# Kernel optimization log

Hardware: AMD Instinct MI355X
Metric: run time of the kernel (lower is better)

The kernel has to match this reference:

```python
import jax, jax.numpy as jnp
import numpy as np

N_NODES = 50000

def cheb_conv(x, edge_index, W, b):
    # PyG ChebConv, K=2, normalization='sym', lambda_max=2.0 (default):
    # scaled Laplacian L_hat = (2/lambda_max)*L - I = -D^{-1/2} A D^{-1/2} (zero diag).
    # Tx_0 = x, Tx_1 = L_hat @ x ; out = Tx_0 @ W[0] + Tx_1 @ W[1] + b
    src, dst = edge_index[0], edge_index[1]
    ones = jnp.ones(src.shape[0], x.dtype)
    deg = jax.ops.segment_sum(ones, src, num_segments=N_NODES)
    dinv = jnp.where(deg > 0, 1.0 / jnp.sqrt(deg), 0.0)
    norm = -dinv[src] * dinv[dst]                                   # [E]
    tx1 = jax.ops.segment_sum(x[src] * norm[:, None], dst, num_segments=N_NODES)
    return x @ W[0] + tx1 @ W[1] + b

def setup_inputs() -> dict:
    key = jax.random.key(0)
    ks = jax.random.split(key, 12)
    IN, OUT, E, P = 128, 2, 800000, 400000
    return {
        "x": jax.random.normal(ks[0], (N_NODES, IN), jnp.float32),
        "edge_index": jax.random.randint(ks[1], (2, E), 0, N_NODES),
        "E_pos": jax.random.randint(ks[2], (2, P), 0, N_NODES),
        "neg_edge_index": jax.random.randint(ks[3], (2, P), 0, N_NODES),
        "W1": jax.random.normal(ks[4], (2, IN, 300), jnp.float32) * 0.05,
        "b1": jnp.zeros((300,), jnp.float32),
        "W2": jax.random.normal(ks[5], (2, 300, 100), jnp.float32) * 0.05,
        "b2": jnp.zeros((100,), jnp.float32),
        "W3": jax.random.normal(ks[6], (2, 100, OUT), jnp.float32) * 0.05,
        "b3": jnp.zeros((OUT,), jnp.float32),
        "lin1_W": jax.random.normal(ks[7], (100, IN), jnp.float32) * 0.05,
        "lin1_b": jnp.zeros((100,), jnp.float32),
        "lin2_W": jax.random.normal(ks[8], (100, IN), jnp.float32) * 0.05,
        "lin2_b": jnp.zeros((100,), jnp.float32),
        "c1": jnp.full((1,), 0.5, jnp.float32),
        "c2": jnp.full((1,), 0.5, jnp.float32),
    }

def reference(x, edge_index, E_pos, neg_edge_index, W1, b1, W2, b2, W3, b3,
              lin1_W, lin1_b, lin2_W, lin2_b, c1, c2):
    # eval mode: F.dropout and dropout_edge are identity
    x0 = x
    h = jax.nn.relu(cheb_conv(x0, edge_index, W1, b1))
    x1 = jax.nn.relu(cheb_conv(h, edge_index, W2, b2))
    x2 = x1 + jax.nn.relu(x0 @ lin1_W.T + lin1_b)
    z = x1 + jax.nn.relu(x0 @ lin2_W.T + lin2_b)
    pos_score = jnp.sum(z[E_pos[0]] * z[E_pos[1]], axis=1)              # [P]
    pos_loss = -jnp.mean(jnp.log(jax.nn.sigmoid(pos_score) + 1e-15))
    neg_score = jnp.sum(z[neg_edge_index[0]] * z[neg_edge_index[1]], axis=1)
    neg_loss = -jnp.mean(jnp.log(1.0 - jax.nn.sigmoid(neg_score) + 1e-15))
    r_loss = pos_loss + neg_loss
    out = cheb_conv(x2, edge_index, W3, b3)                             # [N, out_channels]
    return (out, r_loss, c1, c2)
```

## Files before the change

### kernel.cpp

```cpp
#include <hip/hip_runtime.h>
#include <math.h>


typedef unsigned short ushort_t;
typedef unsigned char u8;
typedef __attribute__((ext_vector_type(8))) __bf16 bf16x8;
typedef __attribute__((ext_vector_type(8))) short s16x8;
typedef __attribute__((ext_vector_type(4))) float f32x4;
typedef __attribute__((ext_vector_type(2))) float f32x2;

#define NB_H 256
#define HW 12500
#define PW 25000
#define LOSS_NB 1792

__device__ __forceinline__ f32x4 mfma16x16x32(s16x8 a, s16x8 b, f32x4 c) {
  return __builtin_amdgcn_mfma_f32_16x16x32_bf16(
      __builtin_bit_cast(bf16x8, a), __builtin_bit_cast(bf16x8, b), c, 0, 0, 0);
}
__device__ __forceinline__ ushort_t f2bf(float f) {
  union { float f; unsigned u; } c; c.f = f;
  unsigned r = (c.u + 0x7FFFu + ((c.u >> 16) & 1u)) >> 16;
  return (ushort_t)r;
}
__device__ __forceinline__ f32x2 cvt2lo(unsigned u) {
  return __builtin_amdgcn_cvt_pk_f32_fp8((int)u, false);
}
__device__ __forceinline__ f32x2 cvt2hi(unsigned u) {
  return __builtin_amdgcn_cvt_pk_f32_fp8((int)u, true);
}
__device__ __forceinline__ u8 f2fp8(float f) {
  return (u8)(__builtin_amdgcn_cvt_pk_fp8_f32(f, 0.f, 0, false) & 0xff);
}

template<int VAR, int NT, int KTOT>
__global__ __launch_bounds__(256) void gemm_mfma(
    const ushort_t* __restrict__ A0, const ushort_t* __restrict__ A1,
    const ushort_t* __restrict__ Wt,
    const float* __restrict__ bias0, const float* __restrict__ bias1,
    const float* __restrict__ x1,
    const float* __restrict__ W3c, const float* __restrict__ b3c,
    void* __restrict__ out0, void* __restrict__ out1,
    float* __restrict__ t0g, float* __restrict__ t1g, int M)
{
  constexpr int NF = NT / 32;
  __shared__ __align__(16) ushort_t As[64 * 40];
  __shared__ __align__(16) ushort_t Bs[NT * 40];
  __shared__ float w3s[400];
  const int tid  = threadIdx.x;
  const int lane = tid & 63, w = tid >> 6;
  const int m0 = blockIdx.x * 64;
  const int wm = (w & 1) * 32, wn = (w >> 1) * (NT / 2);
  if (VAR == 2) { for (int i = tid; i < 400; i += 256) w3s[i] = W3c[i]; }
  f32x4 acc[2][NF];
#pragma unroll
  for (int i = 0; i < 2; ++i)
#pragma unroll
    for (int j = 0; j < NF; ++j) acc[i][j] = (f32x4){0.f, 0.f, 0.f, 0.f};

  for (int k0 = 0; k0 < KTOT; k0 += 32) {
    {
      const int r = tid >> 2, c8 = (tid & 3) * 8;
      const int gm = m0 + r;
      uint4 v = {0u, 0u, 0u, 0u};
      if (gm < M) {
        if (VAR == 1) {
          const u8* s8 = (const u8*)A0 + (size_t)gm * 320 + k0 + c8;
          const uint2 r8 = *(const uint2*)s8;
          const f32x2 f0 = cvt2lo(r8.x), f1 = cvt2hi(r8.x);
          const f32x2 f2 = cvt2lo(r8.y), f3 = cvt2hi(r8.y);
          v.x = (unsigned)f2bf(f0.x) | ((unsigned)f2bf(f0.y) << 16);
          v.y = (unsigned)f2bf(f1.x) | ((unsigned)f2bf(f1.y) << 16);
          v.z = (unsigned)f2bf(f2.x) | ((unsigned)f2bf(f2.y) << 16);
          v.w = (unsigned)f2bf(f3.x) | ((unsigned)f2bf(f3.y) << 16);
        } else {
          const ushort_t* srcp;
          if (VAR == 0) srcp = (k0 < 128) ? A0 + (size_t)gm * 128 + k0 + c8
                                          : A1 + (size_t)gm * 128 + (k0 - 128) + c8;
          else srcp = A0 + (size_t)gm * 128 + k0 + c8;
          v = *(const uint4*)srcp;
        }
      }
      *(uint4*)&As[r * 40 + c8] = v;
    }
    {
      const int c8 = (tid & 3) * 8;
#pragma unroll
      for (int i = 0; i < (NT * 4 + 255) / 256; ++i) {
        const int r = (tid >> 2) + i * 64;
        if (r < NT)
          *(uint4*)&Bs[r * 40 + c8] = *(const uint4*)(Wt + (size_t)r * KTOT + k0 + c8);
      }
    }
    __syncthreads();
    s16x8 af[2], bfr[NF];
#pragma unroll
    for (int mi = 0; mi < 2; ++mi)
      af[mi] = *(const s16x8*)&As[(wm + mi * 16 + (lane & 15)) * 40 + (lane >> 4) * 8];
#pragma unroll
    for (int ni = 0; ni < NF; ++ni)
      bfr[ni] = *(const s16x8*)&Bs[(wn + ni * 16 + (lane & 15)) * 40 + (lane >> 4) * 8];
#pragma unroll
    for (int mi = 0; mi < 2; ++mi)
#pragma unroll
      for (int ni = 0; ni < NF; ++ni)
        acc[mi][ni] = mfma16x16x32(af[mi], bfr[ni], acc[mi][ni]);
    __syncthreads();
  }

  if (VAR == 2) {
#pragma unroll
    for (int mi = 0; mi < 2; ++mi)
#pragma unroll
      for (int r = 0; r < 4; ++r) {
        const int gRow = m0 + wm + mi * 16 + ((lane >> 4) << 2) + r;
        float p0 = 0.f, p1 = 0.f, p2 = 0.f, p3 = 0.f;
#pragma unroll
        for (int ni = 0; ni < NF; ++ni) {
          const int col = wn + ni * 16 + (lane & 15);
          const float v = acc[mi][ni][r];
          if (gRow < M) {
            if (col < 100) {
              const float x2v = x1[(size_t)gRow * 128 + col] + fmaxf(v + bias0[col], 0.f);
              p0 = fmaf(x2v, w3s[col * 2 + 0], p0);
              p1 = fmaf(x2v, w3s[col * 2 + 1], p1);
              p2 = fmaf(x2v, w3s[200 + col * 2 + 0], p2);
              p3 = fmaf(x2v, w3s[200 + col * 2 + 1], p3);
            } else if (col < 200) {
              const int c = col - 100;
              ((u8*)out1)[(size_t)gRow * 128 + c] =
                  f2fp8(x1[(size_t)gRow * 128 + c] + fmaxf(v + bias1[c], 0.f));
            }
          }
        }
        if (wn == 0) {
#pragma unroll
          for (int off = 8; off; off >>= 1) {
            p0 += __shfl_down(p0, off, 16);
            p1 += __shfl_down(p1, off, 16);
            p2 += __shfl_down(p2, off, 16);
            p3 += __shfl_down(p3, off, 16);
          }
          if ((lane & 15) == 0 && gRow < M) {
            t0g[(size_t)gRow * 2 + 0] = p0 + b3c[0];
            t0g[(size_t)gRow * 2 + 1] = p1 + b3c[1];
            t1g[(size_t)gRow * 2 + 0] = p2;
            t1g[(size_t)gRow * 2 + 1] = p3;
          }
        }
      }
  } else {
#pragma unroll
    for (int mi = 0; mi < 2; ++mi)
#pragma unroll
      for (int ni = 0; ni < NF; ++ni)
#pragma unroll
        for (int r = 0; r < 4; ++r) {
          const int gRow = m0 + wm + mi * 16 + ((lane >> 4) << 2) + r;
          const int col  = wn + ni * 16 + (lane & 15);
          if (gRow >= M) continue;
          const float v = acc[mi][ni][r];
          if (VAR == 0) {
            ((u8*)out0)[(size_t)gRow * 320 + col] =
                (col < 300) ? f2fp8(fmaxf(v + bias0[col], 0.f)) : (u8)0;
          } else {
            if (col < 100) ((float*)out0)[(size_t)gRow * 128 + col] = v + bias0[col];
            else if (col < 200) ((u8*)out1)[(size_t)gRow * 128 + (col - 100)] = f2fp8(v);
          }
        }
  }
}

__global__ __launch_bounds__(256) void prep(
    const int* __restrict__ src, const int* __restrict__ dst, int E, int M,
    unsigned* __restrict__ partS, unsigned* __restrict__ partD,
    ushort_t* __restrict__ rank,
    const float* __restrict__ x, ushort_t* __restrict__ xb,
    u8* __restrict__ xf8, int n4,
    const float* __restrict__ W1, const float* __restrict__ W2,
    const float* __restrict__ l1W, const float* __restrict__ l2W,
    ushort_t* __restrict__ W1t, ushort_t* __restrict__ W2t,
    ushort_t* __restrict__ Wlt)
{
  __shared__ unsigned hist[HW];
  const int blk = blockIdx.x;
  if (blk < 512) {
    const int isD = (blk >= 256);
    const int b = isD ? blk - 256 : blk;
    const int* keys = isD ? dst : src;
    unsigned* part = isD ? partD : partS;
    const int cs = (E + NB_H - 1) / NB_H;
    const int e0 = b * cs;
    const int e1 = (e0 + cs < E) ? e0 + cs : E;
    for (int r = 0; r < 2; ++r) {
      const int klo = r * 2 * HW;
      for (int i = threadIdx.x; i < HW; i += 256) hist[i] = 0;
      __syncthreads();
      for (int e = e0 + threadIdx.x; e < e1; e += 256) {
        const int k = keys[e] - klo;
        if ((unsigned)k < (unsigned)(2 * HW)) {
          const unsigned old = atomicAdd(&hist[k >> 1], (k & 1) ? 0x10000u : 1u);
          if (isD) rank[e] = (ushort_t)((old >> ((k & 1) * 16)) & 0xffffu);
        }
      }
      __syncthreads();
      for (int i = threadIdx.x; i < HW; i += 256)
        part[(size_t)b * PW + r * HW + i] = hist[i];
      __syncthreads();
    }
    return;
  }
  const int i = (blk - 512) * 256 + threadIdx.x;
  if (i < n4) {
    const float4 v = ((const float4*)x)[i];
    ushort4 o; o.x = f2bf(v.x); o.y = f2bf(v.y); o.z = f2bf(v.z); o.w = f2bf(v.w);
    ((ushort4*)xb)[i] = o;
    int p = 0;
    p = __builtin_amdgcn_cvt_pk_fp8_f32(v.x, v.y, p, false);
    p = __builtin_amdgcn_cvt_pk_fp8_f32(v.z, v.w, p, true);
    ((unsigned*)xf8)[i] = (unsigned)p;
    return;
  }
  const int j = i - n4;
  if (j < 81920) {
    const int n = j >> 8, k = j & 255;
    float v = 0.f;
    if (n < 300) v = (k < 128) ? W1[k * 300 + n] : W1[38400 + (k - 128) * 300 + n];
    W1t[j] = f2bf(v);
  } else if (j < 153600) {
    const int jj = j - 81920;
    const int n = jj / 320, k = jj - n * 320;
    float v = 0.f;
    if (n < 200 && k < 300) v = W2[(n < 100 ? 0 : 30000) + k * 100 + (n % 100)];
    W2t[jj] = f2bf(v);
  } else if (j < 182272) {
    const int jj = j - 153600;
    const int n = jj >> 7, k = jj & 127;
    float v = 0.f;
    if (n < 100) v = l1W[n * 128 + k];
    else if (n < 200) v = l2W[(n - 100) * 128 + k];
    Wlt[jj] = f2bf(v);
  }
}

__global__ __launch_bounds__(256) void reduce_base2(
    const unsigned* __restrict__ partS, unsigned* __restrict__ partD,
    float* __restrict__ dinv, int* __restrict__ cnt, int M)
{
  const int t = blockIdx.x * 256 + threadIdx.x;
  if (t < PW) {
    const int i = t;
    unsigned ssum = 0;
    for (int b = 0; b < NB_H; b += 8) {
      unsigned v[8];
#pragma unroll
      for (int q = 0; q < 8; ++q) v[q] = partS[(size_t)(b + q) * PW + i];
#pragma unroll
      for (int q = 0; q < 8; ++q) ssum += v[q];
    }
    const int k = 2 * i;
    const unsigned s0 = ssum & 0xffffu, s1 = ssum >> 16;
    if (k < M) dinv[k] = s0 ? 1.f / sqrtf((float)s0) : 0.f;
    if (k + 1 < M) dinv[k + 1] = s1 ? 1.f / sqrtf((float)s1) : 0.f;
  } else if (t < 2 * PW) {
    const int i = t - PW;
    unsigned run = 0;
    for (int b = 0; b < NB_H; b += 8) {
      unsigned v[8], pre[8];
#pragma unroll
      for (int q = 0; q < 8; ++q) v[q] = partD[(size_t)(b + q) * PW + i];
#pragma unroll
      for (int q = 0; q < 8; ++q) { pre[q] = run; run += v[q]; }
#pragma unroll
      for (int q = 0; q < 8; ++q) partD[(size_t)(b + q) * PW + i] = pre[q];
    }
    const int k = 2 * i;
    if (k < M) cnt[k] = (int)(run & 0xffffu);
    if (k + 1 < M) cnt[k + 1] = (int)(run >> 16);
  }
}

__global__ void scan_local(const int* __restrict__ cnt, int* __restrict__ ptr,
                           int* __restrict__ bsum, int n)
{
  __shared__ int tmp[256];
  const int i = blockIdx.x * 256 + threadIdx.x;
  const int v = (i < n) ? cnt[i] : 0;
  tmp[threadIdx.x] = v;
  __syncthreads();
  for (int off = 1; off < 256; off <<= 1) {
    const int t = (threadIdx.x >= off) ? tmp[threadIdx.x - off] : 0;
    __syncthreads();
    tmp[threadIdx.x] += t;
    __syncthreads();
  }
  if (i < n) ptr[i] = tmp[threadIdx.x] - v;
  if (threadIdx.x == 255) bsum[blockIdx.x] = tmp[255];
}
__global__ void scan_add2(int* __restrict__ ptr, const int* __restrict__ bsum,
                          int n, int E, int nb, float* __restrict__ accs)
{
  __shared__ int tmp[256];
  const int v = (threadIdx.x < nb) ? bsum[threadIdx.x] : 0;
  tmp[threadIdx.x] = v;
  __syncthreads();
  for (int off = 1; off < 256; off <<= 1) {
    const int t = (threadIdx.x >= off) ? tmp[threadIdx.x - off] : 0;
    __syncthreads();
    tmp[threadIdx.x] += t;
    __syncthreads();
  }
  __syncthreads();
  const int offset = (blockIdx.x > 0) ? tmp[blockIdx.x - 1] : 0;
  const int i = blockIdx.x * 256 + threadIdx.x;
  if (i < n) ptr[i] += offset;
  if (i == 0) { ptr[n] = E; accs[0] = 0.f; accs[1] = 0.f; }
}

__global__ void fill_csr2(const int* __restrict__ src, const int* __restrict__ dst,
                          const float* __restrict__ dinv, const int* __restrict__ ptr,
                          const unsigned* __restrict__ base32,
                          const ushort_t* __restrict__ rank,
                          int2* __restrict__ csr, int E)
{
  const int e = blockIdx.x * 256 + threadIdx.x;
  if (e >= E) return;
  const int cs = (E + NB_H - 1) / NB_H;
  const int b = e / cs;
  const int s = src[e], d = dst[e];
  const unsigned bv = base32[(size_t)b * PW + (d >> 1)];
  const int base = (int)((bv >> ((d & 1) * 16)) & 0xffffu);
  const int pos = ptr[d] + base + (int)rank[e];
  const float w = -dinv[s] * dinv[d];
  csr[pos] = make_int2(s, __float_as_int(w));
}

#define ACCV(u, ww) { f32x2 t; \
  t = cvt2lo(u.x); a[0]  = fmaf(ww, t.x, a[0]);  a[1]  = fmaf(ww, t.y, a[1]);  \
  t = cvt2hi(u.x); a[2]  = fmaf(ww, t.x, a[2]);  a[3]  = fmaf(ww, t.y, a[3]);  \
  t = cvt2lo(u.y); a[4]  = fmaf(ww, t.x, a[4]);  a[5]  = fmaf(ww, t.y, a[5]);  \
  t = cvt2hi(u.y); a[6]  = fmaf(ww, t.x, a[6]);  a[7]  = fmaf(ww, t.y, a[7]);  \
  t = cvt2lo(u.z); a[8]  = fmaf(ww, t.x, a[8]);  a[9]  = fmaf(ww, t.y, a[9]);  \
  t = cvt2hi(u.z); a[10] = fmaf(ww, t.x, a[10]); a[11] = fmaf(ww, t.y, a[11]); \
  t = cvt2lo(u.w); a[12] = fmaf(ww, t.x, a[12]); a[13] = fmaf(ww, t.y, a[13]); \
  t = cvt2hi(u.w); a[14] = fmaf(ww, t.x, a[14]); a[15] = fmaf(ww, t.y, a[15]); }

__global__ __launch_bounds__(256) void gather128e(
    const u8* __restrict__ xf8, ushort_t* __restrict__ txb,
    const int* __restrict__ ptr, const int2* __restrict__ csr, int M)
{
  const int node = (blockIdx.x * 256 + threadIdx.x) >> 3;
  const int sub  = threadIdx.x & 7;
  if (node >= M) return;
  const int beg = ptr[node], end = ptr[node + 1];
  float a[16] = {};
  int p = beg;
  for (; p + 8 <= end; p += 8) {
    int2 e[8];
#pragma unroll
    for (int q = 0; q < 8; ++q) e[q] = csr[p + q];
    uint4 v[8];
#pragma unroll
    for (int q = 0; q < 8; ++q)
      v[q] = *(const uint4*)(xf8 + (size_t)e[q].x * 128 + sub * 16);
#pragma unroll
    for (int q = 0; q < 8; ++q) { const float wq = __int_as_float(e[q].y); ACCV(v[q], wq) }
  }
  for (; p < end; ++p) {
    const int2 eq = csr[p]; const float wq = __int_as_float(eq.y);
    const uint4 v = *(const uint4*)(xf8 + (size_t)eq.x * 128 + sub * 16);
    ACCV(v, wq)
  }
  uint4 o1, o2;
  o1.x = (unsigned)f2bf(a[0])  | ((unsigned)f2bf(a[1])  << 16);
  o1.y = (unsigned)f2bf(a[2])  | ((unsigned)f2bf(a[3])  << 16);
  o1.z = (unsigned)f2bf(a[4])  | ((unsigned)f2bf(a[5])  << 16);
  o1.w = (unsigned)f2bf(a[6])  | ((unsigned)f2bf(a[7])  << 16);
  o2.x = (unsigned)f2bf(a[8])  | ((unsigned)f2bf(a[9])  << 16);
  o2.y = (unsigned)f2bf(a[10]) | ((unsigned)f2bf(a[11]) << 16);
  o2.z = (unsigned)f2bf(a[12]) | ((unsigned)f2bf(a[13]) << 16);
  o2.w = (unsigned)f2bf(a[14]) | ((unsigned)f2bf(a[15]) << 16);
  ushort_t* dstp = txb + (size_t)node * 128 + sub * 16;
  *(uint4*)dstp = o1;
  *(uint4*)(dstp + 8) = o2;
}

__global__ __launch_bounds__(256) void gather100e_x1(
    const u8* __restrict__ Brh, float* __restrict__ Ar,
    const int* __restrict__ ptr, const int2* __restrict__ csr, int M)
{
  const int node = (blockIdx.x * 256 + threadIdx.x) >> 3;
  const int sub  = threadIdx.x & 7;
  if (node >= M) return;
  const int beg = ptr[node], end = ptr[node + 1];
  float a[16] = {};
  int p = beg;
  for (; p + 8 <= end; p += 8) {
    int2 e[8];
#pragma unroll
    for (int q = 0; q < 8; ++q) e[q] = csr[p + q];
    uint4 v[8];
#pragma unroll
    for (int q = 0; q < 8; ++q)
      v[q] = *(const uint4*)(Brh + (size_t)e[q].x * 128 + sub * 16);
#pragma unroll
    for (int q = 0; q < 8; ++q) { const float wq = __int_as_float(e[q].y); ACCV(v[q], wq) }
  }
  for (; p < end; ++p) {
    const int2 eq = csr[p]; const float wq = __int_as_float(eq.y);
    const uint4 v = *(const uint4*)(Brh + (size_t)eq.x * 128 + sub * 16);
    ACCV(v, wq)
  }
  float* dstp = Ar + (size_t)node * 128 + sub * 16;
#pragma unroll
  for (int q = 0; q < 4; ++q) {
    float4 b = *(const float4*)(dstp + q * 4);
    b.x = fmaxf(b.x + a[q * 4 + 0], 0.f);
    b.y = fmaxf(b.y + a[q * 4 + 1], 0.f);
    b.z = fmaxf(b.z + a[q * 4 + 2], 0.f);
    b.w = fmaxf(b.w + a[q * 4 + 3], 0.f);
    *(float4*)(dstp + q * 4) = b;
  }
}
#undef ACCV

__device__ __forceinline__ void maskrow(uint4& r, int sub) {
  if (sub >= 6) { r.y = 0u; r.z = 0u; r.w = 0u; if (sub == 7) r.x = 0u; }
}
#define DOTV(uu, vv, s) { f32x2 p_, q_; \
  p_ = cvt2lo(uu.x); q_ = cvt2lo(vv.x); s = fmaf(p_.x, q_.x, s); s = fmaf(p_.y, q_.y, s); \
  p_ = cvt2hi(uu.x); q_ = cvt2hi(vv.x); s = fmaf(p_.x, q_.x, s); s = fmaf(p_.y, q_.y, s); \
  p_ = cvt2lo(uu.y); q_ = cvt2lo(vv.y); s = fmaf(p_.x, q_.x, s); s = fmaf(p_.y, q_.y, s); \
  p_ = cvt2hi(uu.y); q_ = cvt2hi(vv.y); s = fmaf(p_.x, q_.x, s); s = fmaf(p_.y, q_.y, s); \
  p_ = cvt2lo(uu.z); q_ = cvt2lo(vv.z); s = fmaf(p_.x, q_.x, s); s = fmaf(p_.y, q_.y, s); \
  p_ = cvt2hi(uu.z); q_ = cvt2hi(vv.z); s = fmaf(p_.x, q_.x, s); s = fmaf(p_.y, q_.y, s); \
  p_ = cvt2lo(uu.w); q_ = cvt2lo(vv.w); s = fmaf(p_.x, q_.x, s); s = fmaf(p_.y, q_.y, s); \
  p_ = cvt2hi(uu.w); q_ = cvt2hi(vv.w); s = fmaf(p_.x, q_.x, s); s = fmaf(p_.y, q_.y, s); }

__global__ __launch_bounds__(256) void loss_g2(
    const u8* __restrict__ zf8, const int* __restrict__ ep,
    const int* __restrict__ en, int P, float* __restrict__ acc,
    const float* __restrict__ t1, const float* __restrict__ t0,
    const int* __restrict__ ptr, const int2* __restrict__ csr,
    float* __restrict__ out, int M)
{
  const int tid = threadIdx.x;
  if (blockIdx.x >= LOSS_NB) {
    const int i = (blockIdx.x - LOSS_NB) * 256 + tid;
    if (i >= M) return;
    float a0 = 0.f, a1 = 0.f;
    const int beg = ptr[i], end = ptr[i + 1];
    int p = beg;
    for (; p + 4 <= end; p += 4) {
      const int2 e0 = csr[p], e1 = csr[p + 1], e2 = csr[p + 2], e3 = csr[p + 3];
      const float w0 = __int_as_float(e0.y), w1 = __int_as_float(e1.y);
      const float w2 = __int_as_float(e2.y), w3 = __int_as_float(e3.y);
      const float2 v0 = *(const float2*)(t1 + (size_t)e0.x * 2);
      const float2 v1 = *(const float2*)(t1 + (size_t)e1.x * 2);
      const float2 v2 = *(const float2*)(t1 + (size_t)e2.x * 2);
      const float2 v3 = *(const float2*)(t1 + (size_t)e3.x * 2);
      a0 = fmaf(w0, v0.x, a0); a1 = fmaf(w0, v0.y, a1);
      a0 = fmaf(w1, v1.x, a0); a1 = fmaf(w1, v1.y, a1);
      a0 = fmaf(w2, v2.x, a0); a1 = fmaf(w2, v2.y, a1);
      a0 = fmaf(w3, v3.x, a0); a1 = fmaf(w3, v3.y, a1);
    }
    for (; p < end; ++p) {
      const int2 eq = csr[p]; const float wq = __int_as_float(eq.y);
      const float2 v = *(const float2*)(t1 + (size_t)eq.x * 2);
      a0 = fmaf(wq, v.x, a0); a1 = fmaf(wq, v.y, a1);
    }
    const float2 base = *(const float2*)(t0 + (size_t)i * 2);
    *(float2*)(out + (size_t)i * 2) = make_float2(base.x + a0, base.y + a1);
    return;
  }
  __shared__ float red[8];
  const int lane = tid & 63, wib = tid >> 6;
  const int sub = tid & 7;
  const int slot0 = blockIdx.x * 32 + (tid >> 3);
  const int step = LOSS_NB * 32;
  float tp = 0.f, tn = 0.f;
  int g = slot0;
  for (; g + 3 * step < 2 * P; g += 4 * step) {
    int neg[4], na[4], nb[4];
#pragma unroll
    for (int q = 0; q < 4; ++q) {
      const int gq = g + q * step;
      neg[q] = (gq >= P);
      const int p = neg[q] ? gq - P : gq;
      const int* ia = neg[q] ? en : ep;
      na[q] = ia[p]; nb[q] = ia[P + p];
    }
    uint4 ra[4], rb[4];
#pragma unroll
    for (int q = 0; q < 4; ++q) {
      ra[q] = make_uint4(0u, 0u, 0u, 0u);
      rb[q] = make_uint4(0u, 0u, 0u, 0u);
      if (sub < 7) {
        ra[q] = *(const uint4*)(zf8 + (size_t)na[q] * 128 + sub * 16);
        rb[q] = *(const uint4*)(zf8 + (size_t)nb[q] * 128 + sub * 16);
      }
      maskrow(ra[q], sub); maskrow(rb[q], sub);
    }
    float s[4] = {0.f, 0.f, 0.f, 0.f};
#pragma unroll
    for (int q = 0; q < 4; ++q) DOTV(ra[q], rb[q], s[q])
#pragma unroll
    for (int off = 4; off; off >>= 1) {
#pragma unroll
      for (int q = 0; q < 4; ++q) s[q] += __shfl_down(s[q], off, 8);
    }
    if (sub == 0) {
#pragma unroll
      for (int q = 0; q < 4; ++q) {
        const float sig = 1.f / (1.f + __expf(-s[q]));
        if (neg[q]) tn += __logf(1.f - sig + 1e-15f); else tp += __logf(sig + 1e-15f);
      }
    }
  }
  for (; g < 2 * P; g += step) {
    const int neg = (g >= P);
    const int p = neg ? g - P : g;
    const int* ia = neg ? en : ep;
    const int na = ia[p], nb = ia[P + p];
    uint4 ra = make_uint4(0u, 0u, 0u, 0u);
    uint4 rb = make_uint4(0u, 0u, 0u, 0u);
    if (sub < 7) {
      ra = *(const uint4*)(zf8 + (size_t)na * 128 + sub * 16);
      rb = *(const uint4*)(zf8 + (size_t)nb * 128 + sub * 16);
    }
    maskrow(ra, sub); maskrow(rb, sub);
    float s = 0.f;
    DOTV(ra, rb, s)
#pragma unroll
    for (int off = 4; off; off >>= 1) s += __shfl_down(s, off, 8);
    if (sub == 0) {
      const float sig = 1.f / (1.f + __expf(-s));
      if (neg) tn += __logf(1.f - sig + 1e-15f); else tp += __logf(sig + 1e-15f);
    }
  }
  tp += __shfl_down(tp, 32, 64); tn += __shfl_down(tn, 32, 64);
  tp += __shfl_down(tp, 16, 64); tn += __shfl_down(tn, 16, 64);
  tp += __shfl_down(tp, 8, 64);  tn += __shfl_down(tn, 8, 64);
  if (lane == 0) { red[wib] = tp; red[4 + wib] = tn; }
  __syncthreads();
  if (tid == 0) {
    atomicAdd(acc + 0, red[0] + red[1] + red[2] + red[3]);
    atomicAdd(acc + 1, red[4] + red[5] + red[6] + red[7]);
  }
}
#undef DOTV

__global__ void final_scalars(const float* __restrict__ accs,
                              const float* __restrict__ c1, const float* __restrict__ c2,
                              float* __restrict__ out, int M, float invP)
{
  out[2 * M + 0] = -(accs[0] + accs[1]) * invP;
  out[2 * M + 1] = c1[0];
  out[2 * M + 2] = c2[0];
}

extern "C" void kernel_launch(void* const* d_in, const int* in_sizes, int n_in,
                              void* d_out, int out_size, void* d_ws, size_t ws_size,
                              hipStream_t stream)
{
  const float* x   = (const float*)d_in[0];
  const int*   ei  = (const int*)d_in[1];
  const int*   ep  = (const int*)d_in[2];
  const int*   en  = (const int*)d_in[3];
  const float* W1  = (const float*)d_in[4];
  const float* b1  = (const float*)d_in[5];
  const float* W2  = (const float*)d_in[6];
  const float* b2  = (const float*)d_in[7];
  const float* W3  = (const float*)d_in[8];
  const float* b3  = (const float*)d_in[9];
  const float* l1W = (const float*)d_in[10];
  const float* l1b = (const float*)d_in[11];
  const float* l2W = (const float*)d_in[12];
  const float* l2b = (const float*)d_in[13];
  const float* c1  = (const float*)d_in[14];
  const float* c2  = (const float*)d_in[15];
  float* out = (float*)d_out;

  const int M = in_sizes[0] / 128;
  const int E = in_sizes[1] / 2;
  const int P = in_sizes[2] / 2;
  const int* src = ei;
  const int* dst = ei + E;
  const int nb_scan = (M + 255) / 256;

  float* ws = (float*)d_ws;
  size_t o = 0;
  float*    dinv = ws + o;            o += 50176;
  int*      cnt  = (int*)(ws + o);    o += (size_t)M;
  int*      ptr  = (int*)(ws + o);    o += (size_t)M + 8;
  int*      bsum = (int*)(ws + o);    o += 256;
  int2*     csr  = (int2*)(ws + o);   o += (size_t)E * 2;
  ushort_t* rank = (ushort_t*)(ws + o); o += (size_t)E / 2;
  ushort_t* xb   = (ushort_t*)(ws + o); o += (size_t)M * 64;
  u8*       xf8  = (u8*)(ws + o);     o += (size_t)M * 32;
  ushort_t* tx0b = (ushort_t*)(ws + o); o += (size_t)M * 64;
  ushort_t* W1t  = (ushort_t*)(ws + o); o += 40960;
  ushort_t* W2t  = (ushort_t*)(ws + o); o += 35840;
  ushort_t* Wlt  = (ushort_t*)(ws + o); o += 14336;
  u8*       h8   = (u8*)(ws + o);     o += (size_t)M * 160;
  float*    Ar   = ws + o;            o += (size_t)M * 128;
  u8*       Brh  = (u8*)(ws + o);     o += (size_t)M * 32;
  u8*       zf8  = (u8*)(ws + o);     o += (size_t)M * 32;
  float*    t0   = ws + o;            o += (size_t)M * 2;
  float*    t1   = ws + o;            o += (size_t)M * 2;
  float*    accs = ws + o;            o += 8;
  unsigned* partS = (unsigned*)h8;
  unsigned* partD = (unsigned*)Ar;

  const int n4 = M * 32;
  const int packBlocks = (n4 + 182272 + 255) / 256;
  prep<<<512 + packBlocks, 256, 0, stream>>>(
      src, dst, E, M, partS, partD, rank,
      x, xb, xf8, n4, W1, W2, l1W, l2W, W1t, W2t, Wlt);

  reduce_base2<<<(2 * PW + 255) / 256, 256, 0, stream>>>(partS, partD, dinv, cnt, M);
  scan_local<<<nb_scan, 256, 0, stream>>>(cnt, ptr, bsum, M);
  scan_add2<<<nb_scan, 256, 0, stream>>>(ptr, bsum, M, E, nb_scan, accs);
  fill_csr2<<<(E + 255) / 256, 256, 0, stream>>>(src, dst, dinv, ptr, partD, rank, csr, E);

  const int gB = (M + 63) / 64;
  const int gE8 = (M * 8 + 255) / 256;

  gather128e<<<gE8, 256, 0, stream>>>(xf8, tx0b, ptr, csr, M);
  gemm_mfma<0, 320, 256><<<gB, 256, 0, stream>>>(
      xb, tx0b, W1t, b1, nullptr, nullptr, nullptr, nullptr, h8, nullptr, nullptr, nullptr, M);

  gemm_mfma<1, 224, 320><<<gB, 256, 0, stream>>>(
      (const ushort_t*)h8, nullptr, W2t, b2, nullptr, nullptr, nullptr, nullptr,
      Ar, Brh, nullptr, nullptr, M);
  gather100e_x1<<<gE8, 256, 0, stream>>>(Brh, Ar, ptr, csr, M);

  gemm_mfma<2, 224, 128><<<gB, 256, 0, stream>>>(
      xb, nullptr, Wlt, l1b, l2b, Ar , W3, b3, nullptr, zf8, t0, t1, M);

  loss_g2<<<LOSS_NB + nb_scan, 256, 0, stream>>>(
      zf8, ep, en, P, accs, t1, t0, ptr, csr, out, M);
  final_scalars<<<1, 1, 0, stream>>>(accs, c1, c2, out, M, 1.0f / (float)P);
}
```

Baseline: 461.4 us.

## Replace per-block LDS histograms with global atomics for degree and CSR ranks

The edge-degree counting switches from per-block shared-memory histograms with partial arrays plus a separate reduce/prefix kernel to direct global atomicAdd on per-node counters, with the returned old value used as the in-bucket rank. The reduce_base2 kernel is removed, dinv computation is folded into scan_local, and fill_csr2 no longer needs the per-block base lookup. A memset is added to zero the counters. The loss kernel also gets an 8-way unrolled gather loop for more memory-level parallelism. Global atomics may contend, and CSR order within a node becomes nondeterministic.

```diff
diff --git a/kernel.cpp b/kernel.cpp
--- a/kernel.cpp
+++ b/kernel.cpp
@@ -9,9 +9,6 @@
 typedef __attribute__((ext_vector_type(4))) float f32x4;
 typedef __attribute__((ext_vector_type(2))) float f32x2;
 
-#define NB_H 256
-#define HW 12500
-#define PW 25000
 #define LOSS_NB 1792
 
 __device__ __forceinline__ f32x4 mfma16x16x32(s16x8 a, s16x8 b, f32x4 c) {
@@ -173,8 +170,8 @@
 
 __global__ __launch_bounds__(256) void prep(
     const int* __restrict__ src, const int* __restrict__ dst, int E, int M,
-    unsigned* __restrict__ partS, unsigned* __restrict__ partD,
-    ushort_t* __restrict__ rank,
+    unsigned* __restrict__ degS, unsigned* __restrict__ cntD,
+    ushort_t* __restrict__ rank, int ebNB,
     const float* __restrict__ x, ushort_t* __restrict__ xb,
     u8* __restrict__ xf8, int n4,
     const float* __restrict__ W1, const float* __restrict__ W2,
@@ -182,35 +179,17 @@
     ushort_t* __restrict__ W1t, ushort_t* __restrict__ W2t,
     ushort_t* __restrict__ Wlt)
 {
-  __shared__ unsigned hist[HW];
   const int blk = blockIdx.x;
-  if (blk < 512) {
-    const int isD = (blk >= 256);
-    const int b = isD ? blk - 256 : blk;
-    const int* keys = isD ? dst : src;
-    unsigned* part = isD ? partD : partS;
-    const int cs = (E + NB_H - 1) / NB_H;
-    const int e0 = b * cs;
-    const int e1 = (e0 + cs < E) ? e0 + cs : E;
-    for (int r = 0; r < 2; ++r) {
-      const int klo = r * 2 * HW;
-      for (int i = threadIdx.x; i < HW; i += 256) hist[i] = 0;
-      __syncthreads();
-      for (int e = e0 + threadIdx.x; e < e1; e += 256) {
-        const int k = keys[e] - klo;
-        if ((unsigned)k < (unsigned)(2 * HW)) {
-          const unsigned old = atomicAdd(&hist[k >> 1], (k & 1) ? 0x10000u : 1u);
-          if (isD) rank[e] = (ushort_t)((old >> ((k & 1) * 16)) & 0xffffu);
-        }
-      }
-      __syncthreads();
-      for (int i = threadIdx.x; i < HW; i += 256)
-        part[(size_t)b * PW + r * HW + i] = hist[i];
-      __syncthreads();
+  if (blk < ebNB) {
+    const int e = blk * 256 + threadIdx.x;
+    if (e < E) {
+      const int s = src[e], d = dst[e];
+      atomicAdd(&degS[s], 1u);
+      rank[e] = (ushort_t)atomicAdd(&cntD[d], 1u);
     }
     return;
   }
-  const int i = (blk - 512) * 256 + threadIdx.x;
+  const int i = (blk - ebNB) * 256 + threadIdx.x;
   if (i < n4) {
     const float4 v = ((const float4*)x)[i];
     ushort4 o; o.x = f2bf(v.x); o.y = f2bf(v.y); o.z = f2bf(v.z); o.w = f2bf(v.w);
@@ -243,49 +222,18 @@
   }
 }
 
-__global__ __launch_bounds__(256) void reduce_base2(
-    const unsigned* __restrict__ partS, unsigned* __restrict__ partD,
-    float* __restrict__ dinv, int* __restrict__ cnt, int M)
-{
-  const int t = blockIdx.x * 256 + threadIdx.x;
-  if (t < PW) {
-    const int i = t;
-    unsigned ssum = 0;
-    for (int b = 0; b < NB_H; b += 8) {
-      unsigned v[8];
-#pragma unroll
-      for (int q = 0; q < 8; ++q) v[q] = partS[(size_t)(b + q) * PW + i];
-#pragma unroll
-      for (int q = 0; q < 8; ++q) ssum += v[q];
-    }
-    const int k = 2 * i;
-    const unsigned s0 = ssum & 0xffffu, s1 = ssum >> 16;
-    if (k < M) dinv[k] = s0 ? 1.f / sqrtf((float)s0) : 0.f;
-    if (k + 1 < M) dinv[k + 1] = s1 ? 1.f / sqrtf((float)s1) : 0.f;
-  } else if (t < 2 * PW) {
-    const int i = t - PW;
-    unsigned run = 0;
-    for (int b = 0; b < NB_H; b += 8) {
-      unsigned v[8], pre[8];
-#pragma unroll
-      for (int q = 0; q < 8; ++q) v[q] = partD[(size_t)(b + q) * PW + i];
-#pragma unroll
-      for (int q = 0; q < 8; ++q) { pre[q] = run; run += v[q]; }
-#pragma unroll
-      for (int q = 0; q < 8; ++q) partD[(size_t)(b + q) * PW + i] = pre[q];
-    }
-    const int k = 2 * i;
-    if (k < M) cnt[k] = (int)(run & 0xffffu);
-    if (k + 1 < M) cnt[k + 1] = (int)(run >> 16);
-  }
-}
-
-__global__ void scan_local(const int* __restrict__ cnt, int* __restrict__ ptr,
-                           int* __restrict__ bsum, int n)
+__global__ void scan_local(const unsigned* __restrict__ cntD,
+                           const unsigned* __restrict__ degS,
+                           float* __restrict__ dinv,
+                           int* __restrict__ ptr, int* __restrict__ bsum, int n)
 {
   __shared__ int tmp[256];
   const int i = blockIdx.x * 256 + threadIdx.x;
-  const int v = (i < n) ? cnt[i] : 0;
+  const int v = (i < n) ? (int)cntD[i] : 0;
+  if (i < n) {
+    const unsigned dg = degS[i];
+    dinv[i] = dg ? 1.f / sqrtf((float)dg) : 0.f;
+  }
   tmp[threadIdx.x] = v;
   __syncthreads();
   for (int off = 1; off < 256; off <<= 1) {
@@ -319,18 +267,13 @@
 
 __global__ void fill_csr2(const int* __restrict__ src, const int* __restrict__ dst,
                           const float* __restrict__ dinv, const int* __restrict__ ptr,
-                          const unsigned* __restrict__ base32,
                           const ushort_t* __restrict__ rank,
                           int2* __restrict__ csr, int E)
 {
   const int e = blockIdx.x * 256 + threadIdx.x;
   if (e >= E) return;
-  const int cs = (E + NB_H - 1) / NB_H;
-  const int b = e / cs;
   const int s = src[e], d = dst[e];
-  const unsigned bv = base32[(size_t)b * PW + (d >> 1)];
-  const int base = (int)((bv >> ((d & 1) * 16)) & 0xffffu);
-  const int pos = ptr[d] + base + (int)rank[e];
+  const int pos = ptr[d] + (int)rank[e];
   const float w = -dinv[s] * dinv[d];
   csr[pos] = make_int2(s, __float_as_int(w));
 }
@@ -480,6 +423,43 @@
   const int step = LOSS_NB * 32;
   float tp = 0.f, tn = 0.f;
   int g = slot0;
+  for (; g + 7 * step < 2 * P; g += 8 * step) {
+    int neg[8], na[8], nb[8];
+#pragma unroll
+    for (int q = 0; q < 8; ++q) {
+      const int gq = g + q * step;
+      neg[q] = (gq >= P);
+      const int p = neg[q] ? gq - P : gq;
+      const int* ia = neg[q] ? en : ep;
+      na[q] = ia[p]; nb[q] = ia[P + p];
+    }
+    uint4 ra[8], rb[8];
+#pragma unroll
+    for (int q = 0; q < 8; ++q) {
+      ra[q] = make_uint4(0u, 0u, 0u, 0u);
+      rb[q] = make_uint4(0u, 0u, 0u, 0u);
+      if (sub < 7) {
+        ra[q] = *(const uint4*)(zf8 + (size_t)na[q] * 128 + sub * 16);
+        rb[q] = *(const uint4*)(zf8 + (size_t)nb[q] * 128 + sub * 16);
+      }
+      maskrow(ra[q], sub); maskrow(rb[q], sub);
+    }
+    float s[8] = {0.f, 0.f, 0.f, 0.f, 0.f, 0.f, 0.f, 0.f};
+#pragma unroll
+    for (int q = 0; q < 8; ++q) DOTV(ra[q], rb[q], s[q])
+#pragma unroll
+    for (int off = 4; off; off >>= 1) {
+#pragma unroll
+      for (int q = 0; q < 8; ++q) s[q] += __shfl_down(s[q], off, 8);
+    }
+    if (sub == 0) {
+#pragma unroll
+      for (int q = 0; q < 8; ++q) {
+        const float sig = 1.f / (1.f + __expf(-s[q]));
+        if (neg[q]) tn += __logf(1.f - sig + 1e-15f); else tp += __logf(sig + 1e-15f);
+      }
+    }
+  }
   for (; g + 3 * step < 2 * P; g += 4 * step) {
     int neg[4], na[4], nb[4];
 #pragma unroll
@@ -587,11 +567,13 @@
   const int* src = ei;
   const int* dst = ei + E;
   const int nb_scan = (M + 255) / 256;
+  const int ebNB = (E + 255) / 256;
 
   float* ws = (float*)d_ws;
   size_t o = 0;
   float*    dinv = ws + o;            o += 50176;
-  int*      cnt  = (int*)(ws + o);    o += (size_t)M;
+  unsigned* degS = (unsigned*)(ws + o); o += (size_t)M;
+  unsigned* cntD = (unsigned*)(ws + o); o += (size_t)M;
   int*      ptr  = (int*)(ws + o);    o += (size_t)M + 8;
   int*      bsum = (int*)(ws + o);    o += 256;
   int2*     csr  = (int2*)(ws + o);   o += (size_t)E * 2;
@@ -609,19 +591,18 @@
   float*    t0   = ws + o;            o += (size_t)M * 2;
   float*    t1   = ws + o;            o += (size_t)M * 2;
   float*    accs = ws + o;            o += 8;
-  unsigned* partS = (unsigned*)h8;
-  unsigned* partD = (unsigned*)Ar;
+
+  hipMemsetAsync(degS, 0, 2 * (size_t)M * sizeof(unsigned), stream);
 
   const int n4 = M * 32;
   const int packBlocks = (n4 + 182272 + 255) / 256;
-  prep<<<512 + packBlocks, 256, 0, stream>>>(
-      src, dst, E, M, partS, partD, rank,
+  prep<<<ebNB + packBlocks, 256, 0, stream>>>(
+      src, dst, E, M, degS, cntD, rank, ebNB,
       x, xb, xf8, n4, W1, W2, l1W, l2W, W1t, W2t, Wlt);
 
-  reduce_base2<<<(2 * PW + 255) / 256, 256, 0, stream>>>(partS, partD, dinv, cnt, M);
-  scan_local<<<nb_scan, 256, 0, stream>>>(cnt, ptr, bsum, M);
+  scan_local<<<nb_scan, 256, 0, stream>>>(cntD, degS, dinv, ptr, bsum, M);
   scan_add2<<<nb_scan, 256, 0, stream>>>(ptr, bsum, M, E, nb_scan, accs);
-  fill_csr2<<<(E + 255) / 256, 256, 0, stream>>>(src, dst, dinv, ptr, partD, rank, csr, E);
+  fill_csr2<<<(E + 255) / 256, 256, 0, stream>>>(src, dst, dinv, ptr, rank, csr, E);
 
   const int gB = (M + 63) / 64;
   const int gE8 = (M * 8 + 255) / 256;
```

After: 488.7 us. 1.06x slower.

## Cut histogram partitions to 64 and fuse partial reduction into local scan

Applied to the files above, without the earlier changes.

Lowers the number of per-block histogram partitions for source and destination degrees from 256 to 64, which shrinks the partial-count arrays that must be written and then reduced. The separate reduce kernel is folded into scan_local: even threads reduce the packed 16-bit counts, write dinv and the per-block rank offsets, and pass totals to the odd lane by shuffle before the block scan. This saves one launch and the cnt round trip through memory. In exchange, the histogram phase has fewer, longer blocks (800000 edges over 64 blocks), and only half the threads in scan_local do the partial-sum loads.

```diff
diff --git a/kernel.cpp b/kernel.cpp
--- a/kernel.cpp
+++ b/kernel.cpp
@@ -9,7 +9,7 @@
 typedef __attribute__((ext_vector_type(4))) float f32x4;
 typedef __attribute__((ext_vector_type(2))) float f32x2;
 
-#define NB_H 256
+#define NB_H 64
 #define HW 12500
 #define PW 25000
 #define LOSS_NB 1792
@@ -184,9 +184,9 @@
 {
   __shared__ unsigned hist[HW];
   const int blk = blockIdx.x;
-  if (blk < 512) {
-    const int isD = (blk >= 256);
-    const int b = isD ? blk - 256 : blk;
+  if (blk < 2 * NB_H) {
+    const int isD = (blk >= NB_H);
+    const int b = isD ? blk - NB_H : blk;
     const int* keys = isD ? dst : src;
     unsigned* part = isD ? partD : partS;
     const int cs = (E + NB_H - 1) / NB_H;
@@ -210,7 +210,7 @@
     }
     return;
   }
-  const int i = (blk - 512) * 256 + threadIdx.x;
+  const int i = (blk - 2 * NB_H) * 256 + threadIdx.x;
   if (i < n4) {
     const float4 v = ((const float4*)x)[i];
     ushort4 o; o.x = f2bf(v.x); o.y = f2bf(v.y); o.z = f2bf(v.z); o.w = f2bf(v.w);
@@ -243,49 +243,45 @@
   }
 }
 
-__global__ __launch_bounds__(256) void reduce_base2(
-    const unsigned* __restrict__ partS, unsigned* __restrict__ partD,
-    float* __restrict__ dinv, int* __restrict__ cnt, int M)
-{
-  const int t = blockIdx.x * 256 + threadIdx.x;
-  if (t < PW) {
-    const int i = t;
-    unsigned ssum = 0;
+__global__ void scan_local(const unsigned* __restrict__ partS,
+                           unsigned* __restrict__ partD,
+                           float* __restrict__ dinv,
+                           int* __restrict__ ptr, int* __restrict__ bsum, int n)
+{
+  __shared__ int tmp[256];
+  const int i = blockIdx.x * 256 + threadIdx.x;
+  const int lane = threadIdx.x & 63;
+  unsigned ssum = 0, dtot = 0;
+  if (i < n && (i & 1) == 0) {
+    const int c = i >> 1;
     for (int b = 0; b < NB_H; b += 8) {
-      unsigned v[8];
-#pragma unroll
-      for (int q = 0; q < 8; ++q) v[q] = partS[(size_t)(b + q) * PW + i];
-#pragma unroll
-      for (int q = 0; q < 8; ++q) ssum += v[q];
-    }
-    const int k = 2 * i;
-    const unsigned s0 = ssum & 0xffffu, s1 = ssum >> 16;
-    if (k < M) dinv[k] = s0 ? 1.f / sqrtf((float)s0) : 0.f;
-    if (k + 1 < M) dinv[k + 1] = s1 ? 1.f / sqrtf((float)s1) : 0.f;
-  } else if (t < 2 * PW) {
-    const int i = t - PW;
+      unsigned sv[8];
+#pragma unroll
+      for (int q = 0; q < 8; ++q) sv[q] = partS[(size_t)(b + q) * PW + c];
+#pragma unroll
+      for (int q = 0; q < 8; ++q) ssum += sv[q];
+    }
     unsigned run = 0;
     for (int b = 0; b < NB_H; b += 8) {
-      unsigned v[8], pre[8];
-#pragma unroll
-      for (int q = 0; q < 8; ++q) v[q] = partD[(size_t)(b + q) * PW + i];
-#pragma unroll
-      for (int q = 0; q < 8; ++q) { pre[q] = run; run += v[q]; }
-#pragma unroll
-      for (int q = 0; q < 8; ++q) partD[(size_t)(b + q) * PW + i] = pre[q];
-    }
-    const int k = 2 * i;
-    if (k < M) cnt[k] = (int)(run & 0xffffu);
-    if (k + 1 < M) cnt[k + 1] = (int)(run >> 16);
-  }
-}
-
-__global__ void scan_local(const int* __restrict__ cnt, int* __restrict__ ptr,
-                           int* __restrict__ bsum, int n)
-{
-  __shared__ int tmp[256];
-  const int i = blockIdx.x * 256 + threadIdx.x;
-  const int v = (i < n) ? cnt[i] : 0;
+      unsigned dv[8];
+#pragma unroll
+      for (int q = 0; q < 8; ++q) dv[q] = partD[(size_t)(b + q) * PW + c];
+#pragma unroll
+      for (int q = 0; q < 8; ++q) { const unsigned pre = run; run += dv[q]; dv[q] = pre; }
+#pragma unroll
+      for (int q = 0; q < 8; ++q) partD[(size_t)(b + q) * PW + c] = dv[q];
+    }
+    dtot = run;
+  }
+  const unsigned sAll = __shfl(ssum, lane & ~1, 64);
+  const unsigned dAll = __shfl(dtot, lane & ~1, 64);
+  int v = 0;
+  if (i < n) {
+    const int hs = (i & 1) * 16;
+    const unsigned dg = (sAll >> hs) & 0xffffu;
+    dinv[i] = dg ? 1.f / sqrtf((float)dg) : 0.f;
+    v = (int)((dAll >> hs) & 0xffffu);
+  }
   tmp[threadIdx.x] = v;
   __syncthreads();
   for (int off = 1; off < 256; off <<= 1) {
@@ -297,6 +293,7 @@
   if (i < n) ptr[i] = tmp[threadIdx.x] - v;
   if (threadIdx.x == 255) bsum[blockIdx.x] = tmp[255];
 }
+
 __global__ void scan_add2(int* __restrict__ ptr, const int* __restrict__ bsum,
                           int n, int E, int nb, float* __restrict__ accs)
 {
@@ -614,12 +611,11 @@
 
   const int n4 = M * 32;
   const int packBlocks = (n4 + 182272 + 255) / 256;
-  prep<<<512 + packBlocks, 256, 0, stream>>>(
+  prep<<<2 * NB_H + packBlocks, 256, 0, stream>>>(
       src, dst, E, M, partS, partD, rank,
       x, xb, xf8, n4, W1, W2, l1W, l2W, W1t, W2t, Wlt);
 
-  reduce_base2<<<(2 * PW + 255) / 256, 256, 0, stream>>>(partS, partD, dinv, cnt, M);
-  scan_local<<<nb_scan, 256, 0, stream>>>(cnt, ptr, bsum, M);
+  scan_local<<<nb_scan, 256, 0, stream>>>(partS, partD, dinv, ptr, bsum, M);
   scan_add2<<<nb_scan, 256, 0, stream>>>(ptr, bsum, M, E, nb_scan, accs);
   fill_csr2<<<(E + 255) / 256, 256, 0, stream>>>(src, dst, dinv, ptr, partD, rank, csr, E);
 
```

Measured after the change: 453.2 us. Within noise of the previous version (-1.8%).
